# Optimization experiments

Measured on AMD Instinct MI355X. Metric: run time of the kernel, lower is better.

## Reference

```python
import jax, jax.numpy as jnp
import numpy as np

N = 50000      # nodes
E = 400000     # edges
IN = 64        # in_channels
HID = 64       # hidden_channels
H = 4          # num_heads
LAT = 32       # latent_dim
NEG_SLOPE = 0.2


def setup_inputs() -> dict:
    key = jax.random.key(0)
    ks = jax.random.split(key, 20)
    w = lambda k, shape, s=0.05: (jax.random.normal(k, shape, jnp.float32) * s)
    inp = {
        'x': jax.random.normal(ks[0], (N, IN), jnp.float32),
        'edge_index': jax.random.randint(ks[1], (2, E), 0, N, dtype=jnp.int32),
        'batch': jnp.zeros((N,), jnp.int32),
        'eps': jax.random.normal(ks[2], (N, LAT), jnp.float32),
        # conv1: in -> HID per head, 4 heads, concat
        'W1': w(ks[3], (IN, H * HID)), 'a_src1': w(ks[4], (H, HID)), 'a_dst1': w(ks[5], (H, HID)), 'b1': jnp.zeros((H * HID,), jnp.float32),
        # conv2: H*HID -> HID per head, concat
        'W2': w(ks[6], (H * HID, H * HID)), 'a_src2': w(ks[7], (H, HID)), 'a_dst2': w(ks[8], (H, HID)), 'b2': jnp.zeros((H * HID,), jnp.float32),
        # conv_mu / conv_logvar: H*HID -> LAT, 1 head, no concat
        'Wmu': w(ks[9], (H * HID, LAT)), 'a_src_mu': w(ks[10], (1, LAT)), 'a_dst_mu': w(ks[11], (1, LAT)), 'b_mu': jnp.zeros((LAT,), jnp.float32),
        'Wlv': w(ks[12], (H * HID, LAT)), 'a_src_lv': w(ks[13], (1, LAT)), 'a_dst_lv': w(ks[14], (1, LAT)), 'b_lv': jnp.zeros((LAT,), jnp.float32),
        # decoder
        'W_fc': w(ks[15], (LAT, HID)), 'b_fc': jnp.zeros((HID,), jnp.float32),
        'W_node': w(ks[16], (HID, IN)), 'b_node': jnp.zeros((IN,), jnp.float32),
        'W_edge': w(ks[17], (HID, 1)), 'b_edge': jnp.zeros((1,), jnp.float32),
    }
    return inp


def gat_layer(x, W, a_src, a_dst, b, src, dst, concat):
    """PyG-style GATConv: gather -> leaky_relu score -> per-dst softmax -> scatter-add."""
    n = x.shape[0]
    heads, c = a_src.shape
    h = (x @ W).reshape(n, heads, c)                     # [N,H,C]
    s_src = jnp.einsum('nhc,hc->nh', h, a_src)           # [N,H]
    s_dst = jnp.einsum('nhc,hc->nh', h, a_dst)
    e = jax.nn.leaky_relu(s_src[src] + s_dst[dst], NEG_SLOPE)   # [E,H]
    m = jax.ops.segment_max(e, dst, num_segments=n)      # stable softmax per destination
    e = jnp.exp(e - m[dst])
    denom = jax.ops.segment_sum(e, dst, num_segments=n)
    alpha = e / (denom[dst] + 1e-16)                     # [E,H]
    out = jax.ops.segment_sum(alpha[:, :, None] * h[src], dst, num_segments=n)  # [N,H,C]
    out = out.reshape(n, heads * c) if concat else out.mean(axis=1)
    return out + b


def reference(x, edge_index, batch, eps,
              W1, a_src1, a_dst1, b1,
              W2, a_src2, a_dst2, b2,
              Wmu, a_src_mu, a_dst_mu, b_mu,
              Wlv, a_src_lv, a_dst_lv, b_lv,
              W_fc, b_fc, W_node, b_node, W_edge, b_edge):
    n = x.shape[0]
    src0, dst0 = edge_index[0], edge_index[1]
    loops = jnp.arange(n, dtype=edge_index.dtype)        # GATConv add_self_loops=True
    src = jnp.concatenate([src0, loops])
    dst = jnp.concatenate([dst0, loops])

    # encode
    h = jax.nn.relu(gat_layer(x, W1, a_src1, a_dst1, b1, src, dst, concat=True))
    h = jax.nn.relu(gat_layer(h, W2, a_src2, a_dst2, b2, src, dst, concat=True))
    mu = gat_layer(h, Wmu, a_src_mu, a_dst_mu, b_mu, src, dst, concat=False)
    logvar = gat_layer(h, Wlv, a_src_lv, a_dst_lv, b_lv, src, dst, concat=False)

    # reparameterize (eps supplied for determinism)
    z = mu + eps * jnp.exp(0.5 * logvar)

    # decode
    zd = jax.nn.relu(z @ W_fc + b_fc)                    # [N,HID]
    node_features = zd @ W_node + b_node                 # [N,IN]
    edge_feat = zd[src0] * zd[dst0]                      # [E,HID]
    edge_scores = (edge_feat @ W_edge + b_edge).squeeze(-1)  # [E]
    return (mu, logvar, z, node_features, edge_scores)
```

## Files before the change

kernel.cpp:

```cpp
#include <hip/hip_runtime.h>
#include <math.h>

#define NEG_SLOPE 0.2f

__device__ __forceinline__ float lky(float x){ return x > 0.f ? x : NEG_SLOPE * x; }

__device__ __forceinline__ unsigned short f2bf(float f){
  unsigned int u = __float_as_uint(f);
  unsigned int r = (u + 0x7fffu + ((u >> 16) & 1u)) >> 16;
  return (unsigned short)r;
}
__device__ __forceinline__ float bf2f(unsigned short s){
  return __uint_as_float(((unsigned int)s) << 16);
}
__device__ __forceinline__ void unp8(uint4 v, float* f){
  f[0]=__uint_as_float(v.x<<16); f[1]=__uint_as_float(v.x&0xffff0000u);
  f[2]=__uint_as_float(v.y<<16); f[3]=__uint_as_float(v.y&0xffff0000u);
  f[4]=__uint_as_float(v.z<<16); f[5]=__uint_as_float(v.z&0xffff0000u);
  f[6]=__uint_as_float(v.w<<16); f[7]=__uint_as_float(v.w&0xffff0000u);
}
__device__ __forceinline__ uint4 pack8(const float* o){
  uint4 v;
  v.x = (unsigned)f2bf(o[0]) | ((unsigned)f2bf(o[1])<<16);
  v.y = (unsigned)f2bf(o[2]) | ((unsigned)f2bf(o[3])<<16);
// ... 2 lines not shown
  return v;
}

typedef __bf16 bf16x8 __attribute__((ext_vector_type(8)));
typedef float  f32x4  __attribute__((ext_vector_type(4)));
typedef float  f32x2  __attribute__((ext_vector_type(2)));

__device__ __forceinline__ uint2 pk_fp8(const float* f){
  unsigned lo = 0u, hi = 0u;
  lo = __builtin_amdgcn_cvt_pk_fp8_f32(f[0], f[1], (int)lo, false);
  lo = __builtin_amdgcn_cvt_pk_fp8_f32(f[2], f[3], (int)lo, true);
  hi = __builtin_amdgcn_cvt_pk_fp8_f32(f[4], f[5], (int)hi, false);
  hi = __builtin_amdgcn_cvt_pk_fp8_f32(f[6], f[7], (int)hi, true);
  return make_uint2(lo, hi);
}
__device__ __forceinline__ unsigned pk_fp8x4(float f0, float f1, float f2, float f3){
  unsigned u = 0u;
  u = __builtin_amdgcn_cvt_pk_fp8_f32(f0, f1, (int)u, false);
  u = __builtin_amdgcn_cvt_pk_fp8_f32(f2, f3, (int)u, true);
  return u;
}
__device__ __forceinline__ void unpk_fp8(uint2 v, float* f){
  f32x2 a0 = __builtin_amdgcn_cvt_pk_f32_fp8((int)v.x, false);
  f32x2 a1 = __builtin_amdgcn_cvt_pk_f32_fp8((int)v.x, true);
  f32x2 a2 = __builtin_amdgcn_cvt_pk_f32_fp8((int)v.y, false);
  f32x2 a3 = __builtin_amdgcn_cvt_pk_f32_fp8((int)v.y, true);
  f[0]=a0[0]; f[1]=a0[1]; f[2]=a1[0]; f[3]=a1[1];
  f[4]=a2[0]; f[5]=a2[1]; f[6]=a3[0]; f[7]=a3[1];
}

__global__ void zero_ints_kernel(int* __restrict__ p, int n){
  int i = blockIdx.x * blockDim.x + threadIdx.x;
  if (i < n) p[i] = 0;
}
__global__ void count_deg_kernel(const int* __restrict__ dst, int* __restrict__ deg, int E){
  int e = blockIdx.x * blockDim.x + threadIdx.x;
  if (e < E) atomicAdd(&deg[dst[e]], 1);
}
__global__ void scan_chunk_kernel(const int* __restrict__ deg, int* __restrict__ rowptr,
                                  int* __restrict__ bsum, int n){
  __shared__ int s[256];
  int t = threadIdx.x;
  int i = blockIdx.x * 256 + t;
  int v = (i < n) ? deg[i] : 0;
  s[t] = v; __syncthreads();
  for (int off = 1; off < 256; off <<= 1){
    int x = (t >= off) ? s[t - off] : 0;
    __syncthreads();
    s[t] += x;
    __syncthreads();
  }
  if (i < n) rowptr[i + 1] = s[t];
  if (t == 255) bsum[blockIdx.x] = s[255];
}
__global__ void scan_add_kernel(int* __restrict__ rowptr, const int* __restrict__ bsum,
                                int nb, int n){
  __shared__ int s[256];
  int t = threadIdx.x;
  int v = (t < nb) ? bsum[t] : 0;
  s[t] = v; __syncthreads();
  for (int off = 1; off < 256; off <<= 1){
    int x = (t >= off) ? s[t - off] : 0;
    __syncthreads();
    s[t] += x;
    __syncthreads();
  }
  int b = blockIdx.x;
  int excl = (b == 0) ? 0 : s[b - 1];
  int i = b * 256 + t;
  if (i < n) rowptr[i + 1] += excl;
  if (i == 0) rowptr[0] = 0;
}
__global__ void fill_csr_kernel(const int* __restrict__ src, const int* __restrict__ dst,
                                const int* __restrict__ rowptr, int* __restrict__ cursor,
                                int* __restrict__ colv, int E){
  int e = blockIdx.x * blockDim.x + threadIdx.x;
  if (e >= E) return;
  int d = dst[e];
  int pos = atomicAdd(&cursor[d], 1);
  colv[rowptr[d] + pos] = src[e];
}

__device__ __forceinline__ void pack_one(const float* Wa, const float* Wb,
                                         int K, int M, int Mhalf,
                                         unsigned short* out, int idx){
  if (idx >= K * M) return;
  int j = idx & 7;
  int l = (idx >> 3) & 63;
  int rest = idx >> 9;
  int KS = K >> 5;
  int s = rest % KS, gct = rest / KS;
  int col = gct * 16 + (l & 15);
  int k   = s * 32 + ((l >> 4) << 3) + j;
  float v;
  if (Wb == nullptr) v = Wa[(long)k * M + col];
  else v = (col < Mhalf) ? Wa[(long)k * Mhalf + col] : Wb[(long)k * Mhalf + (col - Mhalf)];
  out[idx] = f2bf(v);
}

__global__ __launch_bounds__(256) void packall_kernel(
    const float* __restrict__ W1,  unsigned short* __restrict__ W1pk,
    const float* __restrict__ W2,  unsigned short* __restrict__ W2pk,
    const float* __restrict__ Wmu, const float* __restrict__ Wlv,
    unsigned short* __restrict__ Wmvpk,
    const float* __restrict__ Wfc, unsigned short* __restrict__ Wfcpk,
    const float* __restrict__ Wnd, unsigned short* __restrict__ Wndpk,
    const float* __restrict__ as1, const float* __restrict__ ad1,
    float* __restrict__ P1)
{
  int b = blockIdx.x, t = threadIdx.x;
  if (b < 64){
    pack_one(W1, nullptr, 64, 256, 256, W1pk, b * 256 + t);
  } else if (b < 320){
    pack_one(W2, nullptr, 256, 256, 256, W2pk, (b - 64) * 256 + t);
  } else if (b < 384){
    pack_one(Wmu, Wlv, 256, 64, 32, Wmvpk, (b - 320) * 256 + t);
  } else if (b < 392){
    pack_one(Wfc, nullptr, 32, 64, 64, Wfcpk, (b - 384) * 256 + t);
  } else if (b < 408){
    pack_one(Wnd, nullptr, 64, 64, 64, Wndpk, (b - 392) * 256 + t);
  } else {
    int idx = (b - 408) * 256 + t;
    if (idx < 512){
      int sd = idx & 1, h = (idx >> 1) & 3, k = idx >> 3;
      const float* av = sd ? ad1 : as1;
      float acc = 0.f;
      for (int c = 0; c < 64; ++c) acc += W1[k * 256 + h * 64 + c] * av[h * 64 + c];
      P1[idx] = acc;
    }
  }
}

__global__ __launch_bounds__(256) void score1cvt_kernel(
    const float* __restrict__ x, const float* __restrict__ P1,
    unsigned short* __restrict__ xb,
    float* __restrict__ S1s, float* __restrict__ S1d, int n)
{
  __shared__ float P[512];
  int t = threadIdx.x;
  P[t] = P1[t]; P[t + 256] = P1[t + 256];
  __syncthreads();
  int nid = blockIdx.x * 256 + t;
  if (nid >= n) return;
  const float4* xr = (const float4*)x + (long)nid * 16;
  uint4* xw = (uint4*)xb + (long)nid * 8;
  float acc[8] = {0,0,0,0,0,0,0,0};
  for (int kc = 0; kc < 16; kc += 2){
    float4 v0 = xr[kc], v1 = xr[kc + 1];
    uint4 o;
    o.x = (unsigned)f2bf(v0.x) | ((unsigned)f2bf(v0.y) << 16);
    o.y = (unsigned)f2bf(v0.z) | ((unsigned)f2bf(v0.w) << 16);
    o.z = (unsigned)f2bf(v1.x) | ((unsigned)f2bf(v1.y) << 16);
    o.w = (unsigned)f2bf(v1.z) | ((unsigned)f2bf(v1.w) << 16);
    xw[kc >> 1] = o;
    float vf[8] = {v0.x, v0.y, v0.z, v0.w, v1.x, v1.y, v1.z, v1.w};
    #pragma unroll
    for (int j = 0; j < 8; ++j){
      int k = kc * 4 + j;
      #pragma unroll
      for (int o8 = 0; o8 < 8; ++o8) acc[o8] += vf[j] * P[k * 8 + o8];
    }
  }
  *(float4*)(S1s + nid * 4) = make_float4(acc[0], acc[2], acc[4], acc[6]);
  *(float4*)(S1d + nid * 4) = make_float4(acc[1], acc[3], acc[5], acc[7]);
}

__global__ __launch_bounds__(256) void aggx_kernel(
    const unsigned short* __restrict__ xb,
    const float* __restrict__ Ss, const float* __restrict__ Sd,
    const int* __restrict__ rowptr, const int* __restrict__ colv,
    unsigned short* __restrict__ Xagg, int n)
{
  int wv = threadIdx.x >> 6, l = threadIdx.x & 63;
  int nid = blockIdx.x * 4 + wv;
  if (nid >= n) return;
  int slot = l >> 5;
  int cl = l & 31;
  float4 sdv = *(const float4*)(Sd + (long)nid * 4);
  float acc[4][2] = {};
  float sumw[4] = {0.f, 0.f, 0.f, 0.f};
  int beg = rowptr[nid], end = rowptr[nid + 1];
  for (int jj = beg + slot; jj < end; jj += 2){
    int s = colv[jj];
    float4 a = *(const float4*)(Ss + (long)s * 4);
    float wx = __expf(lky(a.x + sdv.x));
    float wy = __expf(lky(a.y + sdv.y));
    float wz = __expf(lky(a.z + sdv.z));
    float ww = __expf(lky(a.w + sdv.w));
    unsigned xv = *((const unsigned*)xb + (long)s * 32 + cl);
    float f0 = __uint_as_float(xv << 16);
    float f1 = __uint_as_float(xv & 0xffff0000u);
    acc[0][0] += wx * f0; acc[0][1] += wx * f1;
    acc[1][0] += wy * f0; acc[1][1] += wy * f1;
    acc[2][0] += wz * f0; acc[2][1] += wz * f1;
    acc[3][0] += ww * f0; acc[3][1] += ww * f1;
    sumw[0] += wx; sumw[1] += wy; sumw[2] += wz; sumw[3] += ww;
  }
  #pragma unroll
  for (int h = 0; h < 4; ++h){
    acc[h][0] += __shfl_xor(acc[h][0], 32);
    acc[h][1] += __shfl_xor(acc[h][1], 32);
    sumw[h]   += __shfl_xor(sumw[h], 32);
  }
  float4 ssv = *(const float4*)(Ss + (long)nid * 4);
  unsigned xv = *((const unsigned*)xb + (long)nid * 32 + cl);
  float f0 = __uint_as_float(xv << 16);
  float f1 = __uint_as_float(xv & 0xffff0000u);
  float wsh[4] = { __expf(lky(ssv.x + sdv.x)), __expf(lky(ssv.y + sdv.y)),
                   __expf(lky(ssv.z + sdv.z)), __expf(lky(ssv.w + sdv.w)) };
  if (l < 32){
    #pragma unroll
    for (int h = 0; h < 4; ++h){
      float inv = 1.f / (sumw[h] + wsh[h] + 1e-16f);
      float o0 = (acc[h][0] + wsh[h] * f0) * inv;
      float o1 = (acc[h][1] + wsh[h] * f1) * inv;
      unsigned ov = (unsigned)f2bf(o0) | ((unsigned)f2bf(o1) << 16);
      *((unsigned*)Xagg + (long)nid * 128 + h * 32 + cl) = ov;
    }
  }
}

template<int K, int KB, int CW, bool BD, bool SCORES, bool RELU, bool OUT8>
__global__ __launch_bounds__(256) void gemm_mfma_kernel(
    const unsigned short* __restrict__ Xb, const unsigned short* __restrict__ Wpk,
    const float* __restrict__ a_s, const float* __restrict__ a_d,
    const float* __restrict__ a_s2, const float* __restrict__ a_d2,
    const float* __restrict__ bias,
    void* __restrict__ Hout,
    float* __restrict__ Ss, float* __restrict__ Sd,
    float* __restrict__ Ss2, float* __restrict__ Sd2, int n)
{
  constexpr int BR  = (CW == 4) ? 32 : 128;
  constexpr int M   = 64 * CW;
  constexpr int KSB = KB / 32;
  constexpr int LDA = K + 8;
  constexpr int SH  = (BR * LDA > BR * M) ? BR * LDA : BR * M;
  __shared__ unsigned short As[SH];

  const int t = threadIdx.x;
  const int w = t >> 6, l = t & 63;
  const int quad = l >> 4, l15 = l & 15;
  const long base = (long)blockIdx.x * BR;
  const int roww = (CW == 4) ? 0 : w;
  const int colw = (CW == 4) ? w : 0;
  const int abase = BD ? w * KB : 0;

  {
    const uint4* Xg = (const uint4*)Xb;
    long g0 = base * (K / 8);
    long lim = (long)n * (K / 8);
    for (int c = t; c < BR * K / 8; c += 256){
      int row = c / (K / 8), kc = c % (K / 8);
      uint4 v = make_uint4(0u, 0u, 0u, 0u);
      if (g0 + c < lim) v = Xg[g0 + c];
      *(uint4*)(As + row * LDA + kc * 8) = v;
    }
  }
  __syncthreads();

  f32x4 acc[2][4] = {};
  for (int s = 0; s < KSB; ++s){
    bf16x8 af0 = *(const bf16x8*)(As + (roww * 32 + 0  + l15) * LDA + abase + s * 32 + quad * 8);
    bf16x8 af1 = *(const bf16x8*)(As + (roww * 32 + 16 + l15) * LDA + abase + s * 32 + quad * 8);
    #pragma unroll
    for (int ct = 0; ct < 4; ++ct){
      int gct = colw * 4 + ct;
      bf16x8 bf = *(const bf16x8*)(Wpk + (((long)gct * KSB + s) * 64 + l) * 8);
      acc[0][ct] = __builtin_amdgcn_mfma_f32_16x16x32_bf16(af0, bf, acc[0][ct], 0, 0, 0);
      acc[1][ct] = __builtin_amdgcn_mfma_f32_16x16x32_bf16(af1, bf, acc[1][ct], 0, 0, 0);
    }
  }

  if constexpr (SCORES){
    if (CW == 4){
      const int head = w;
      float asv[4], adv[4];
      #pragma unroll
      for (int ct = 0; ct < 4; ++ct){
        int col = head * 64 + ct * 16 + l15;
        asv[ct] = a_s[col]; adv[ct] = a_d[col];
      }
      #pragma unroll
      for (int rt = 0; rt < 2; ++rt){
        #pragma unroll
        for (int r = 0; r < 4; ++r){
          float ps = 0.f, pd = 0.f;
          #pragma unroll
          for (int ct = 0; ct < 4; ++ct){
            float v = acc[rt][ct][r];
            ps += v * asv[ct]; pd += v * adv[ct];
          }
          ps += __shfl_xor(ps, 8); pd += __shfl_xor(pd, 8);
          ps += __shfl_xor(ps, 4); pd += __shfl_xor(pd, 4);
          ps += __shfl_xor(ps, 2); pd += __shfl_xor(pd, 2);
          ps += __shfl_xor(ps, 1); pd += __shfl_xor(pd, 1);
          long node = base + rt * 16 + quad * 4 + r;
          if (l15 == 0 && node < n){ Ss[node * 4 + head] = ps; Sd[node * 4 + head] = pd; }
        }
      }
    } else {
      float asm_[2], adm_[2], asl_[2], adl_[2];
      #pragma unroll
      for (int ct = 0; ct < 2; ++ct){
        int col = ct * 16 + l15;
        asm_[ct] = a_s[col];  adm_[ct] = a_d[col];
        asl_[ct] = a_s2[col]; adl_[ct] = a_d2[col];
      }
      #pragma unroll
      for (int rt = 0; rt < 2; ++rt){
        #pragma unroll
        for (int r = 0; r < 4; ++r){
          float psm = 0.f, pdm = 0.f, psl = 0.f, pdl = 0.f;
          #pragma unroll
          for (int ct = 0; ct < 2; ++ct){
            float vm = acc[rt][ct][r];
            float vl = acc[rt][ct + 2][r];
            psm += vm * asm_[ct]; pdm += vm * adm_[ct];
            psl += vl * asl_[ct]; pdl += vl * adl_[ct];
          }
          #pragma unroll
          for (int d = 8; d >= 1; d >>= 1){
            psm += __shfl_xor(psm, d); pdm += __shfl_xor(pdm, d);
            psl += __shfl_xor(psl, d); pdl += __shfl_xor(pdl, d);
          }
          long node = base + w * 32 + rt * 16 + quad * 4 + r;
          if (l15 == 0 && node < n){
            Ss[node]  = psm; Sd[node]  = pdm;
            Ss2[node] = psl; Sd2[node] = pdl;
          }
        }
      }
    }
  }

  __syncthreads();
  float bct[4] = {0.f, 0.f, 0.f, 0.f};
  if constexpr (RELU){
    #pragma unroll
    for (int ct = 0; ct < 4; ++ct) bct[ct] = bias[colw * 64 + ct * 16 + l15];
  }
  #pragma unroll
  for (int rt = 0; rt < 2; ++rt){
    #pragma unroll
    for (int ct = 0; ct < 4; ++ct){
      #pragma unroll
      for (int r = 0; r < 4; ++r){
        int row = roww * 32 + rt * 16 + quad * 4 + r;
        int col = colw * 64 + ct * 16 + l15;
        float o = acc[rt][ct][r];
        if constexpr (RELU) o = fmaxf(o + bct[ct], 0.f);
        int pos = col;
        if constexpr (CW == 1){ pos = (col < 32) ? (col * 2) : ((col - 32) * 2 + 1); }
        As[row * M + pos] = f2bf(o);
      }
    }
  }
  __syncthreads();
  if constexpr (OUT8){
    uint2* Hg = (uint2*)Hout;
    for (int c = t; c < BR * M / 8; c += 256){
      int row = c / (M / 8);
      uint4 v = *(const uint4*)(As + c * 8);
      float f[8]; unp8(v, f);
      if (base + row < n) Hg[base * (M / 8) + c] = pk_fp8(f);
    }
  } else {
    uint4* Hg = (uint4*)Hout;
    for (int c = t; c < BR * M / 8; c += 256){
      int row = c / (M / 8);
      if (base + row < n) Hg[base * (M / 8) + c] = *(const uint4*)(As + c * 8);
    }
  }
}

__global__ __launch_bounds__(256) void agg256_kernel(
    const unsigned char* __restrict__ H8,
    const float* __restrict__ Ss, const float* __restrict__ Sd,
    const int* __restrict__ rowptr, const int* __restrict__ colv,
    const float* __restrict__ bias, unsigned short* __restrict__ Out, int n)
{
  int wv = threadIdx.x >> 6, l = threadIdx.x & 63;
  int nid = blockIdx.x * 4 + wv;
  if (nid >= n) return;
  int slot = l >> 5;
  int cl = l & 31;
  int head = cl >> 3;
  float sdv = Sd[(long)nid * 4 + head];
  const uint2* H8v = (const uint2*)H8;
  float acc[8] = {0,0,0,0,0,0,0,0};
  float sumw = 0.f;
  int beg = rowptr[nid], end = rowptr[nid + 1];
  for (int jj = beg + slot; jj < end; jj += 2){
    int s = colv[jj];
    float wt = __expf(lky(Ss[(long)s * 4 + head] + sdv));
    uint2 hv = H8v[(long)s * 32 + cl];
    float xf[8]; unpk_fp8(hv, xf);
    #pragma unroll
    for (int j = 0; j < 8; ++j) acc[j] += wt * xf[j];
    sumw += wt;
  }
  #pragma unroll
  for (int j = 0; j < 8; ++j) acc[j] += __shfl_xor(acc[j], 32);
  sumw += __shfl_xor(sumw, 32);
  float wself = __expf(lky(Ss[(long)nid * 4 + head] + sdv));
  uint2 hv = H8v[(long)nid * 32 + cl];
  float xf[8]; unpk_fp8(hv, xf);
  if (l < 32){
    float inv = 1.f / (sumw + wself + 1e-16f);
    float4 bv0 = *(const float4*)(bias + cl * 8);
    float4 bv1 = *(const float4*)(bias + cl * 8 + 4);
    float o[8];
    o[0] = fmaxf((acc[0] + wself * xf[0]) * inv + bv0.x, 0.f);
    o[1] = fmaxf((acc[1] + wself * xf[1]) * inv + bv0.y, 0.f);
    o[2] = fmaxf((acc[2] + wself * xf[2]) * inv + bv0.z, 0.f);
    o[3] = fmaxf((acc[3] + wself * xf[3]) * inv + bv0.w, 0.f);
    o[4] = fmaxf((acc[4] + wself * xf[4]) * inv + bv1.x, 0.f);
    o[5] = fmaxf((acc[5] + wself * xf[5]) * inv + bv1.y, 0.f);
    o[6] = fmaxf((acc[6] + wself * xf[6]) * inv + bv1.z, 0.f);
    o[7] = fmaxf((acc[7] + wself * xf[7]) * inv + bv1.w, 0.f);
    *((uint4*)Out + (long)nid * 32 + cl) = pack8(o);
  }
}

__global__ __launch_bounds__(256) void agg_muv_kernel(
    const unsigned short* __restrict__ Hmuv,
    const float* __restrict__ Ssm, const float* __restrict__ Sdm,
    const float* __restrict__ Ssl, const float* __restrict__ Sdl,
    const int* __restrict__ rowptr, const int* __restrict__ colv,
    const float* __restrict__ bmu, const float* __restrict__ blv,
    const float* __restrict__ epsv,
    float* __restrict__ out_mu, float* __restrict__ out_lv, float* __restrict__ out_z,
    unsigned short* __restrict__ zb, int n)
{
  int wv = threadIdx.x >> 6, l = threadIdx.x & 63;
  int nid = blockIdx.x * 4 + wv;
  if (nid >= n) return;
  int slot = l >> 5;
  int cl = l & 31;
  float sdm = Sdm[nid], sdl = Sdl[nid];
  const unsigned* Hm32 = (const unsigned*)Hmuv;
  float am = 0.f, al = 0.f, summ = 0.f, suml = 0.f;
  int beg = rowptr[nid], end = rowptr[nid + 1];
  for (int jj = beg + slot; jj < end; jj += 2){
    int s = colv[jj];
    float wm = __expf(lky(Ssm[s] + sdm));
    float wl = __expf(lky(Ssl[s] + sdl));
    unsigned hv = Hm32[(long)s * 32 + cl];
    float mu = __uint_as_float(hv << 16);
    float lv = __uint_as_float(hv & 0xffff0000u);
    am += wm * mu; al += wl * lv;
    summ += wm; suml += wl;
  }
  am += __shfl_xor(am, 32); al += __shfl_xor(al, 32);
  summ += __shfl_xor(summ, 32); suml += __shfl_xor(suml, 32);
  float wms = __expf(lky(Ssm[nid] + sdm));
  float wls = __expf(lky(Ssl[nid] + sdl));
  unsigned hv = Hm32[(long)nid * 32 + cl];
  float mus = __uint_as_float(hv << 16);
  float lvs = __uint_as_float(hv & 0xffff0000u);
  if (l < 32){
    float mu = (am + wms * mus) / (summ + wms + 1e-16f) + bmu[cl];
    float lv = (al + wls * lvs) / (suml + wls + 1e-16f) + blv[cl];
    float z  = mu + epsv[(long)nid * 32 + cl] * expf(0.5f * lv);
    out_mu[(long)nid * 32 + cl] = mu;
    out_lv[(long)nid * 32 + cl] = lv;
    out_z [(long)nid * 32 + cl] = z;
    zb[(long)nid * 32 + cl] = f2bf(z);
  }
}

__global__ __launch_bounds__(256) void decoder_mfma_kernel(
    const unsigned short* __restrict__ zb,
    const unsigned short* __restrict__ Wfcpk, const float* __restrict__ bfc,
    const unsigned short* __restrict__ Wndpk, const float* __restrict__ bnode,
    unsigned char* __restrict__ ZD8, float* __restrict__ NF, int n)
{
  constexpr int LDA = 40;
  constexpr int LDZ = 72;
  __shared__ unsigned short As[128 * LDA];
  __shared__ unsigned short Zs[128 * LDZ];
  const int t = threadIdx.x;
  const int w = t >> 6, l = t & 63;
  const int quad = l >> 4, l15 = l & 15;
  const long base = (long)blockIdx.x * 128;

  {
    const uint4* Zg = (const uint4*)zb;
    long g0 = base * 4;
    long lim = (long)n * 4;
    for (int c = t; c < 512; c += 256){
      int row = c >> 2, kc = c & 3;
      uint4 v = make_uint4(0u, 0u, 0u, 0u);
      if (g0 + c < lim) v = Zg[g0 + c];
      *(uint4*)(As + row * LDA + kc * 8) = v;
    }
  }
  __syncthreads();

  f32x4 acc[2][4] = {};
  {
// ... 99 lines not shown
  const float* W2    = (const float*)d_in[8];
  const float* as2   = (const float*)d_in[9];
  const float* ad2   = (const float*)d_in[10];
  const float* b2    = (const float*)d_in[11];
  const float* Wmu   = (const float*)d_in[12];
  const float* asmu  = (const float*)d_in[13];
  const float* admu  = (const float*)d_in[14];
  const float* bmu   = (const float*)d_in[15];
  const float* Wlv   = (const float*)d_in[16];
  const float* aslv  = (const float*)d_in[17];
  const float* adlv  = (const float*)d_in[18];
  const float* blv   = (const float*)d_in[19];
  const float* Wfc   = (const float*)d_in[20];
  const float* bfc   = (const float*)d_in[21];
  const float* Wnode = (const float*)d_in[22];
  const float* bnode = (const float*)d_in[23];
  const float* Wedge = (const float*)d_in[24];
  const float* bedge = (const float*)d_in[25];

  const int N = in_sizes[0] / 64;
  const int E = in_sizes[1] / 2;
  const int* srcA = ei;
  const int* dstA = ei + E;

  char* wsb = (char*)d_ws;
  size_t off = 0;
  auto alloc = [&](size_t bytes) -> void* {
    void* p = wsb + off;
    off += (bytes + 255) & ~(size_t)255;
    return p;
  };
  unsigned short* xb    = (unsigned short*)alloc((size_t)N * 64 * 2);
  unsigned short* bufP  = (unsigned short*)alloc((size_t)N * 256 * 2);
  unsigned short* bufQ  = (unsigned short*)alloc((size_t)N * 256 * 2);
  unsigned char*  H8    = (unsigned char*) alloc((size_t)N * 256);
  unsigned short* Hmuv  = (unsigned short*)alloc((size_t)N * 64 * 2);
  unsigned char*  ZD8   = (unsigned char*) alloc((size_t)N * 64);
  unsigned short* zbb   = (unsigned short*)alloc((size_t)N * 32 * 2);
  unsigned short* W1pk  = (unsigned short*)alloc((size_t)64 * 256 * 2);
  unsigned short* W2pk  = (unsigned short*)alloc((size_t)256 * 256 * 2);
  unsigned short* Wmvpk = (unsigned short*)alloc((size_t)256 * 64 * 2);
  unsigned short* Wfcpk = (unsigned short*)alloc((size_t)32 * 64 * 2);
  unsigned short* Wndpk = (unsigned short*)alloc((size_t)64 * 64 * 2);
  float* P1    = (float*)alloc(512 * 4);
  float* S1s   = (float*)alloc((size_t)N * 4 * 4);
  float* S1d   = (float*)alloc((size_t)N * 4 * 4);
  float* S2s   = (float*)alloc((size_t)N * 4 * 4);
  float* S2d   = (float*)alloc((size_t)N * 4 * 4);
  float* Ssm   = (float*)alloc((size_t)N * 4);
  float* Sdm   = (float*)alloc((size_t)N * 4);
  float* Ssl   = (float*)alloc((size_t)N * 4);
  float* Sdl   = (float*)alloc((size_t)N * 4);
  int*   deg   = (int*)  alloc((size_t)N * 2 * 4);
  int*   cursor= deg + N;
  int*   rowptr= (int*)  alloc((size_t)(N + 1) * 4);
  int*   colv  = (int*)  alloc((size_t)E * 4);
  int*   bsum  = (int*)  alloc(1024);
  (void)ws_size; (void)n_in; (void)out_size;

  float* out_mu = (float*)d_out;
  float* out_lv = out_mu + (size_t)N * 32;
  float* out_z  = out_lv + (size_t)N * 32;
  float* out_nf = out_z  + (size_t)N * 32;
  float* out_es = out_nf + (size_t)N * 64;

  const int nb = (N + 255) / 256;

  zero_ints_kernel<<<(2 * N + 255) / 256, 256, 0, stream>>>(deg, 2 * N);
  count_deg_kernel<<<(E + 255) / 256, 256, 0, stream>>>(dstA, deg, E);
  scan_chunk_kernel<<<nb, 256, 0, stream>>>(deg, rowptr, bsum, N);
  scan_add_kernel<<<nb, 256, 0, stream>>>(rowptr, bsum, nb, N);
  fill_csr_kernel<<<(E + 255) / 256, 256, 0, stream>>>(srcA, dstA, rowptr, cursor, colv, E);

  packall_kernel<<<410, 256, 0, stream>>>(W1, W1pk, W2, W2pk, Wmu, Wlv, Wmvpk,
                                          Wfc, Wfcpk, Wnode, Wndpk, as1, ad1, P1);

  score1cvt_kernel<<<(N + 255) / 256, 256, 0, stream>>>(x, P1, xb, S1s, S1d, N);
  aggx_kernel<<<(N + 3) / 4, 256, 0, stream>>>(xb, S1s, S1d, rowptr, colv, bufP, N);
  gemm_mfma_kernel<256, 64, 4, true, false, true, false><<<(N + 31) / 32, 256, 0, stream>>>(
      bufP, W1pk, nullptr, nullptr, nullptr, nullptr, b1, bufQ,
      nullptr, nullptr, nullptr, nullptr, N);

  gemm_mfma_kernel<256, 256, 4, false, true, false, true><<<(N + 31) / 32, 256, 0, stream>>>(
      bufQ, W2pk, as2, ad2, nullptr, nullptr, nullptr, H8,
      S2s, S2d, nullptr, nullptr, N);
  agg256_kernel<<<(N + 3) / 4, 256, 0, stream>>>(H8, S2s, S2d, rowptr, colv, b2, bufP, N);

  gemm_mfma_kernel<256, 256, 1, false, true, false, false><<<(N + 127) / 128, 256, 0, stream>>>(
      bufP, Wmvpk, asmu, admu, aslv, adlv, nullptr, Hmuv,
      Ssm, Sdm, Ssl, Sdl, N);
  agg_muv_kernel<<<(N + 3) / 4, 256, 0, stream>>>(
      Hmuv, Ssm, Sdm, Ssl, Sdl, rowptr, colv, bmu, blv, epsv,
      out_mu, out_lv, out_z, zbb, N);

  decoder_mfma_kernel<<<(N + 127) / 128, 256, 0, stream>>>(
      zbb, Wfcpk, bfc, Wndpk, bnode, ZD8, out_nf, N);
  {
    long waves = ((long)E + 7) / 8;
    long blocks = (waves + 3) / 4;
    edge_score_kernel<<<(int)blocks, 256, 0, stream>>>(ZD8, srcA, dstA, Wedge, bedge, out_es, E);
  }
}
```

Measured before the change: 354.3 us.

## Fuse setup kernels, fuse layer-1/layer-2 GEMMs, widen aggregation lanes

Degree counting, weight packing, P1 projection and the x conversion/scoring are merged into one launch, and cursor zeroing moves into scan_add. The two layer GEMMs become one kernel that keeps the relu(XW1+b1) tile in LDS, so the bufQ round trip through global memory goes away. The aggregation kernels now use 4 edge slots of 16 lanes with wider loads instead of 2 slots of 32 lanes. This cuts launches and memory traffic, at the cost of recomputing P1 in every scoring block and adding extra shuffle reductions.

```diff
diff --git a/kernel.cpp b/kernel.cpp
--- a/kernel.cpp
+++ b/kernel.cpp
@@ -58,10 +58,6 @@
 __global__ void zero_ints_kernel(int* __restrict__ p, int n){
   int i = blockIdx.x * blockDim.x + threadIdx.x;
   if (i < n) p[i] = 0;
-}
-__global__ void count_deg_kernel(const int* __restrict__ dst, int* __restrict__ deg, int E){
-  int e = blockIdx.x * blockDim.x + threadIdx.x;
-  if (e < E) atomicAdd(&deg[dst[e]], 1);
 }
 __global__ void scan_chunk_kernel(const int* __restrict__ deg, int* __restrict__ rowptr,
                                   int* __restrict__ bsum, int n){
@@ -80,7 +76,7 @@
   if (t == 255) bsum[blockIdx.x] = s[255];
 }
 __global__ void scan_add_kernel(int* __restrict__ rowptr, const int* __restrict__ bsum,
-                                int nb, int n){
+                                int* __restrict__ cursor, int nb, int n){
   __shared__ int s[256];
   int t = threadIdx.x;
   int v = (t < nb) ? bsum[t] : 0;
@@ -94,7 +90,7 @@
   int b = blockIdx.x;
   int excl = (b == 0) ? 0 : s[b - 1];
   int i = b * 256 + t;
-  if (i < n) rowptr[i + 1] += excl;
+  if (i < n){ rowptr[i + 1] += excl; cursor[i] = 0; }
   if (i == 0) rowptr[0] = 0;
 }
 __global__ void fill_csr_kernel(const int* __restrict__ src, const int* __restrict__ dst,
@@ -124,7 +120,8 @@
   out[idx] = f2bf(v);
 }
 
-__global__ __launch_bounds__(256) void packall_kernel(
+__global__ __launch_bounds__(256) void mega_kernel(
+    const int* __restrict__ dstA, int* __restrict__ deg, int E, int nbE,
     const float* __restrict__ W1,  unsigned short* __restrict__ W1pk,
     const float* __restrict__ W2,  unsigned short* __restrict__ W2pk,
     const float* __restrict__ Wmu, const float* __restrict__ Wlv,
@@ -132,41 +129,37 @@
     const float* __restrict__ Wfc, unsigned short* __restrict__ Wfcpk,
     const float* __restrict__ Wnd, unsigned short* __restrict__ Wndpk,
     const float* __restrict__ as1, const float* __restrict__ ad1,
-    float* __restrict__ P1)
+    const float* __restrict__ x, unsigned short* __restrict__ xb,
+    float* __restrict__ S1s, float* __restrict__ S1d, int n)
 {
   int b = blockIdx.x, t = threadIdx.x;
-  if (b < 64){
-    pack_one(W1, nullptr, 64, 256, 256, W1pk, b * 256 + t);
-  } else if (b < 320){
-    pack_one(W2, nullptr, 256, 256, 256, W2pk, (b - 64) * 256 + t);
-  } else if (b < 384){
-    pack_one(Wmu, Wlv, 256, 64, 32, Wmvpk, (b - 320) * 256 + t);
-  } else if (b < 392){
-    pack_one(Wfc, nullptr, 32, 64, 64, Wfcpk, (b - 384) * 256 + t);
-  } else if (b < 408){
-    pack_one(Wnd, nullptr, 64, 64, 64, Wndpk, (b - 392) * 256 + t);
-  } else {
-    int idx = (b - 408) * 256 + t;
-    if (idx < 512){
-      int sd = idx & 1, h = (idx >> 1) & 3, k = idx >> 3;
-      const float* av = sd ? ad1 : as1;
-      float acc = 0.f;
-      for (int c = 0; c < 64; ++c) acc += W1[k * 256 + h * 64 + c] * av[h * 64 + c];
-      P1[idx] = acc;
-    }
-  }
-}
-
-__global__ __launch_bounds__(256) void score1cvt_kernel(
-    const float* __restrict__ x, const float* __restrict__ P1,
-    unsigned short* __restrict__ xb,
-    float* __restrict__ S1s, float* __restrict__ S1d, int n)
-{
+  if (b < nbE){
+    int e = b * 256 + t;
+    if (e < E) atomicAdd(&deg[dstA[e]], 1);
+    return;
+  }
+  b -= nbE;
+  if (b < 408){
+    if (b < 64)       pack_one(W1, nullptr, 64, 256, 256, W1pk, b * 256 + t);
+    else if (b < 320) pack_one(W2, nullptr, 256, 256, 256, W2pk, (b - 64) * 256 + t);
+    else if (b < 384) pack_one(Wmu, Wlv, 256, 64, 32, Wmvpk, (b - 320) * 256 + t);
+    else if (b < 392) pack_one(Wfc, nullptr, 32, 64, 64, Wfcpk, (b - 384) * 256 + t);
+    else              pack_one(Wnd, nullptr, 64, 64, 64, Wndpk, (b - 392) * 256 + t);
+    return;
+  }
+  b -= 408;
   __shared__ float P[512];
-  int t = threadIdx.x;
-  P[t] = P1[t]; P[t + 256] = P1[t + 256];
+  #pragma unroll
+  for (int rep = 0; rep < 2; ++rep){
+    int idx = t + rep * 256;
+    int sd = idx & 1, h = (idx >> 1) & 3, k = idx >> 3;
+    const float* av = sd ? ad1 : as1;
+    float acc = 0.f;
+    for (int c = 0; c < 64; ++c) acc += W1[k * 256 + h * 64 + c] * av[h * 64 + c];
+    P[idx] = acc;
+  }
   __syncthreads();
-  int nid = blockIdx.x * 256 + t;
+  int nid = b * 256 + t;
   if (nid >= n) return;
   const float4* xr = (const float4*)x + (long)nid * 16;
   uint4* xw = (uint4*)xb + (long)nid * 8;
@@ -200,49 +193,235 @@
   int wv = threadIdx.x >> 6, l = threadIdx.x & 63;
   int nid = blockIdx.x * 4 + wv;
   if (nid >= n) return;
-  int slot = l >> 5;
-  int cl = l & 31;
+  int slot = l >> 4;
+  int cl = l & 15;
   float4 sdv = *(const float4*)(Sd + (long)nid * 4);
-  float acc[4][2] = {};
+  const uint2* xb2 = (const uint2*)xb;
+  float acc[4][4] = {};
   float sumw[4] = {0.f, 0.f, 0.f, 0.f};
   int beg = rowptr[nid], end = rowptr[nid + 1];
-  for (int jj = beg + slot; jj < end; jj += 2){
+  for (int jj = beg + slot; jj < end; jj += 4){
     int s = colv[jj];
     float4 a = *(const float4*)(Ss + (long)s * 4);
     float wx = __expf(lky(a.x + sdv.x));
     float wy = __expf(lky(a.y + sdv.y));
     float wz = __expf(lky(a.z + sdv.z));
     float ww = __expf(lky(a.w + sdv.w));
-    unsigned xv = *((const unsigned*)xb + (long)s * 32 + cl);
-    float f0 = __uint_as_float(xv << 16);
-    float f1 = __uint_as_float(xv & 0xffff0000u);
-    acc[0][0] += wx * f0; acc[0][1] += wx * f1;
-    acc[1][0] += wy * f0; acc[1][1] += wy * f1;
-    acc[2][0] += wz * f0; acc[2][1] += wz * f1;
-    acc[3][0] += ww * f0; acc[3][1] += ww * f1;
+    uint2 xv = xb2[(long)s * 16 + cl];
+    float f0 = __uint_as_float(xv.x << 16);
+    float f1 = __uint_as_float(xv.x & 0xffff0000u);
+    float f2 = __uint_as_float(xv.y << 16);
+    float f3 = __uint_as_float(xv.y & 0xffff0000u);
+    acc[0][0] += wx*f0; acc[0][1] += wx*f1; acc[0][2] += wx*f2; acc[0][3] += wx*f3;
+    acc[1][0] += wy*f0; acc[1][1] += wy*f1; acc[1][2] += wy*f2; acc[1][3] += wy*f3;
+    acc[2][0] += wz*f0; acc[2][1] += wz*f1; acc[2][2] += wz*f2; acc[2][3] += wz*f3;
+    acc[3][0] += ww*f0; acc[3][1] += ww*f1; acc[3][2] += ww*f2; acc[3][3] += ww*f3;
     sumw[0] += wx; sumw[1] += wy; sumw[2] += wz; sumw[3] += ww;
   }
   #pragma unroll
-  for (int h = 0; h < 4; ++h){
-    acc[h][0] += __shfl_xor(acc[h][0], 32);
-    acc[h][1] += __shfl_xor(acc[h][1], 32);
-    sumw[h]   += __shfl_xor(sumw[h], 32);
+  for (int d = 16; d <= 32; d <<= 1){
+    #pragma unroll
+    for (int h = 0; h < 4; ++h){
+      #pragma unroll
+      for (int j = 0; j < 4; ++j) acc[h][j] += __shfl_xor(acc[h][j], d);
+      sumw[h] += __shfl_xor(sumw[h], d);
+    }
   }
   float4 ssv = *(const float4*)(Ss + (long)nid * 4);
-  unsigned xv = *((const unsigned*)xb + (long)nid * 32 + cl);
-  float f0 = __uint_as_float(xv << 16);
-  float f1 = __uint_as_float(xv & 0xffff0000u);
+  uint2 xv = xb2[(long)nid * 16 + cl];
+  float f0 = __uint_as_float(xv.x << 16);
+  float f1 = __uint_as_float(xv.x & 0xffff0000u);
+  float f2 = __uint_as_float(xv.y << 16);
+  float f3 = __uint_as_float(xv.y & 0xffff0000u);
   float wsh[4] = { __expf(lky(ssv.x + sdv.x)), __expf(lky(ssv.y + sdv.y)),
                    __expf(lky(ssv.z + sdv.z)), __expf(lky(ssv.w + sdv.w)) };
-  if (l < 32){
+  if (l < 16){
+    uint2* Xo = (uint2*)Xagg;
     #pragma unroll
     for (int h = 0; h < 4; ++h){
       float inv = 1.f / (sumw[h] + wsh[h] + 1e-16f);
       float o0 = (acc[h][0] + wsh[h] * f0) * inv;
       float o1 = (acc[h][1] + wsh[h] * f1) * inv;
-      unsigned ov = (unsigned)f2bf(o0) | ((unsigned)f2bf(o1) << 16);
-      *((unsigned*)Xagg + (long)nid * 128 + h * 32 + cl) = ov;
-    }
+      float o2 = (acc[h][2] + wsh[h] * f2) * inv;
+      float o3 = (acc[h][3] + wsh[h] * f3) * inv;
+      uint2 ov;
+      ov.x = (unsigned)f2bf(o0) | ((unsigned)f2bf(o1) << 16);
+      ov.y = (unsigned)f2bf(o2) | ((unsigned)f2bf(o3) << 16);
+      Xo[(long)nid * 64 + h * 16 + cl] = ov;
+    }
+  }
+}
+
+__global__ __launch_bounds__(256) void gemm12_kernel(
+    const unsigned short* __restrict__ Xagg,
+    const unsigned short* __restrict__ W1pk, const unsigned short* __restrict__ W2pk,
+    const float* __restrict__ b1,
+    const float* __restrict__ a_s, const float* __restrict__ a_d,
+    unsigned char* __restrict__ H8,
+    float* __restrict__ Ss, float* __restrict__ Sd, int n)
+{
+  constexpr int LDA = 264;
+  __shared__ unsigned short As[32 * LDA];
+  __shared__ unsigned short Bs[32 * LDA];
+  const int t = threadIdx.x;
+  const int w = t >> 6, l = t & 63;
+  const int quad = l >> 4, l15 = l & 15;
+  const long base = (long)blockIdx.x * 32;
+
+  {
+    const uint4* Xg = (const uint4*)Xagg;
+    long g0 = base * 32;
+    long lim = (long)n * 32;
+    for (int c = t; c < 1024; c += 256){
+      int row = c >> 5, kc = c & 31;
+      uint4 v = make_uint4(0u, 0u, 0u, 0u);
+      if (g0 + c < lim) v = Xg[g0 + c];
+      *(uint4*)(As + row * LDA + kc * 8) = v;
+    }
+  }
+  __syncthreads();
+
+  f32x4 acc1[2][4] = {};
+  const int abase = w * 64;
+  #pragma unroll
+  for (int s = 0; s < 2; ++s){
+    bf16x8 af0 = *(const bf16x8*)(As + (0  + l15) * LDA + abase + s * 32 + quad * 8);
+    bf16x8 af1 = *(const bf16x8*)(As + (16 + l15) * LDA + abase + s * 32 + quad * 8);
+    #pragma unroll
+    for (int ct = 0; ct < 4; ++ct){
+      int gct = w * 4 + ct;
+      bf16x8 bf = *(const bf16x8*)(W1pk + (((long)gct * 2 + s) * 64 + l) * 8);
+      acc1[0][ct] = __builtin_amdgcn_mfma_f32_16x16x32_bf16(af0, bf, acc1[0][ct], 0, 0, 0);
+      acc1[1][ct] = __builtin_amdgcn_mfma_f32_16x16x32_bf16(af1, bf, acc1[1][ct], 0, 0, 0);
+    }
+  }
+  #pragma unroll
+  for (int rt = 0; rt < 2; ++rt){
+    #pragma unroll
+    for (int ct = 0; ct < 4; ++ct){
+      float b = b1[w * 64 + ct * 16 + l15];
+      #pragma unroll
+      for (int r = 0; r < 4; ++r){
+        int row = rt * 16 + quad * 4 + r;
+        Bs[row * LDA + w * 64 + ct * 16 + l15] = f2bf(fmaxf(acc1[rt][ct][r] + b, 0.f));
+      }
+    }
+  }
+  __syncthreads();
+
+  f32x4 acc[2][4] = {};
+  for (int s = 0; s < 8; ++s){
+    bf16x8 af0 = *(const bf16x8*)(Bs + (0  + l15) * LDA + s * 32 + quad * 8);
+    bf16x8 af1 = *(const bf16x8*)(Bs + (16 + l15) * LDA + s * 32 + quad * 8);
+    #pragma unroll
+    for (int ct = 0; ct < 4; ++ct){
+      int gct = w * 4 + ct;
+      bf16x8 bf = *(const bf16x8*)(W2pk + (((long)gct * 8 + s) * 64 + l) * 8);
+      acc[0][ct] = __builtin_amdgcn_mfma_f32_16x16x32_bf16(af0, bf, acc[0][ct], 0, 0, 0);
+      acc[1][ct] = __builtin_amdgcn_mfma_f32_16x16x32_bf16(af1, bf, acc[1][ct], 0, 0, 0);
+    }
+  }
+
+  {
+    float asv[4], adv[4];
+    #pragma unroll
+    for (int ct = 0; ct < 4; ++ct){
+      int col = w * 64 + ct * 16 + l15;
+      asv[ct] = a_s[col]; adv[ct] = a_d[col];
+    }
+    #pragma unroll
+    for (int rt = 0; rt < 2; ++rt){
+      #pragma unroll
+      for (int r = 0; r < 4; ++r){
+        float ps = 0.f, pd = 0.f;
+        #pragma unroll
+        for (int ct = 0; ct < 4; ++ct){
+          float v = acc[rt][ct][r];
+          ps += v * asv[ct]; pd += v * adv[ct];
+        }
+        ps += __shfl_xor(ps, 8); pd += __shfl_xor(pd, 8);
+        ps += __shfl_xor(ps, 4); pd += __shfl_xor(pd, 4);
+        ps += __shfl_xor(ps, 2); pd += __shfl_xor(pd, 2);
+        ps += __shfl_xor(ps, 1); pd += __shfl_xor(pd, 1);
+        long node = base + rt * 16 + quad * 4 + r;
+        if (l15 == 0 && node < n){ Ss[node * 4 + w] = ps; Sd[node * 4 + w] = pd; }
+      }
+    }
+  }
+
+  #pragma unroll
+  for (int rt = 0; rt < 2; ++rt){
+    #pragma unroll
+    for (int ct = 0; ct < 4; ++ct){
+      #pragma unroll
+      for (int r = 0; r < 4; ++r){
+        int row = rt * 16 + quad * 4 + r;
+        As[row * 256 + w * 64 + ct * 16 + l15] = f2bf(acc[rt][ct][r]);
+      }
+    }
+  }
+  __syncthreads();
+  {
+    uint2* Hg = (uint2*)H8;
+    for (int c = t; c < 1024; c += 256){
+      int row = c >> 5;
+      uint4 v = *(const uint4*)(As + c * 8);
+      float f[8]; unp8(v, f);
+      if (base + row < n) Hg[base * 32 + c] = pk_fp8(f);
+    }
+  }
+}
+
+__global__ __launch_bounds__(256) void agg256_kernel(
+    const unsigned char* __restrict__ H8,
+    const float* __restrict__ Ss, const float* __restrict__ Sd,
+    const int* __restrict__ rowptr, const int* __restrict__ colv,
+    const float* __restrict__ bias, unsigned short* __restrict__ Out, int n)
+{
+  int wv = threadIdx.x >> 6, l = threadIdx.x & 63;
+  int nid = blockIdx.x * 4 + wv;
+  if (nid >= n) return;
+  int slot = l >> 4;
+  int cl = l & 15;
+  int head = cl >> 2;
+  float sdv = Sd[(long)nid * 4 + head];
+  const uint4* H8v = (const uint4*)H8;
+  float acc[16] = {0,0,0,0,0,0,0,0,0,0,0,0,0,0,0,0};
+  float sumw = 0.f;
+  int beg = rowptr[nid], end = rowptr[nid + 1];
+  for (int jj = beg + slot; jj < end; jj += 4){
+    int s = colv[jj];
+    float wt = __expf(lky(Ss[(long)s * 4 + head] + sdv));
+    uint4 hv = H8v[(long)s * 16 + cl];
+    float xf[16];
+    unpk_fp8(make_uint2(hv.x, hv.y), xf);
+    unpk_fp8(make_uint2(hv.z, hv.w), xf + 8);
+    #pragma unroll
+    for (int j = 0; j < 16; ++j) acc[j] += wt * xf[j];
+    sumw += wt;
+  }
+  #pragma unroll
+  for (int d = 16; d <= 32; d <<= 1){
+    #pragma unroll
+    for (int j = 0; j < 16; ++j) acc[j] += __shfl_xor(acc[j], d);
+    sumw += __shfl_xor(sumw, d);
+  }
+  float wself = __expf(lky(Ss[(long)nid * 4 + head] + sdv));
+  uint4 hv = H8v[(long)nid * 16 + cl];
+  float xf[16];
+  unpk_fp8(make_uint2(hv.x, hv.y), xf);
+  unpk_fp8(make_uint2(hv.z, hv.w), xf + 8);
+  if (l < 16){
+    float inv = 1.f / (sumw + wself + 1e-16f);
+    float o[16];
+    #pragma unroll
+    for (int j = 0; j < 16; ++j){
+      float b = bias[cl * 16 + j];
+      o[j] = fmaxf((acc[j] + wself * xf[j]) * inv + b, 0.f);
+    }
+    uint4* Og = (uint4*)Out;
+    Og[(long)nid * 32 + cl * 2]     = pack8(o);
+    Og[(long)nid * 32 + cl * 2 + 1] = pack8(o + 8);
   }
 }
 
@@ -298,73 +477,40 @@
   }
 
   if constexpr (SCORES){
-    if (CW == 4){
-      const int head = w;
-      float asv[4], adv[4];
+    float asm_[2], adm_[2], asl_[2], adl_[2];
+    #pragma unroll
+    for (int ct = 0; ct < 2; ++ct){
+      int col = ct * 16 + l15;
+      asm_[ct] = a_s[col];  adm_[ct] = a_d[col];
+      asl_[ct] = a_s2[col]; adl_[ct] = a_d2[col];
+    }
+    #pragma unroll
+    for (int rt = 0; rt < 2; ++rt){
       #pragma unroll
-      for (int ct = 0; ct < 4; ++ct){
-        int col = head * 64 + ct * 16 + l15;
-        asv[ct] = a_s[col]; adv[ct] = a_d[col];
-      }
-      #pragma unroll
-      for (int rt = 0; rt < 2; ++rt){
+      for (int r = 0; r < 4; ++r){
+        float psm = 0.f, pdm = 0.f, psl = 0.f, pdl = 0.f;
         #pragma unroll
-        for (int r = 0; r < 4; ++r){
-          float ps = 0.f, pd = 0.f;
-          #pragma unroll
-          for (int ct = 0; ct < 4; ++ct){
-            float v = acc[rt][ct][r];
-            ps += v * asv[ct]; pd += v * adv[ct];
-          }
-          ps += __shfl_xor(ps, 8); pd += __shfl_xor(pd, 8);
-          ps += __shfl_xor(ps, 4); pd += __shfl_xor(pd, 4);
-          ps += __shfl_xor(ps, 2); pd += __shfl_xor(pd, 2);
-          ps += __shfl_xor(ps, 1); pd += __shfl_xor(pd, 1);
-          long node = base + rt * 16 + quad * 4 + r;
-          if (l15 == 0 && node < n){ Ss[node * 4 + head] = ps; Sd[node * 4 + head] = pd; }
+        for (int ct = 0; ct < 2; ++ct){
+          float vm = acc[rt][ct][r];
+          float vl = acc[rt][ct + 2][r];
+          psm += vm * asm_[ct]; pdm += vm * adm_[ct];
+          psl += vl * asl_[ct]; pdl += vl * adl_[ct];
+        }
+        #pragma unroll
+        for (int d = 8; d >= 1; d >>= 1){
+          psm += __shfl_xor(psm, d); pdm += __shfl_xor(pdm, d);
+          psl += __shfl_xor(psl, d); pdl += __shfl_xor(pdl, d);
+        }
+        long node = base + w * 32 + rt * 16 + quad * 4 + r;
+        if (l15 == 0 && node < n){
+          Ss[node]  = psm; Sd[node]  = pdm;
+          Ss2[node] = psl; Sd2[node] = pdl;
         }
       }
-    } else {
-      float asm_[2], adm_[2], asl_[2], adl_[2];
-      #pragma unroll
-      for (int ct = 0; ct < 2; ++ct){
-        int col = ct * 16 + l15;
-        asm_[ct] = a_s[col];  adm_[ct] = a_d[col];
-        asl_[ct] = a_s2[col]; adl_[ct] = a_d2[col];
-      }
-      #pragma unroll
-      for (int rt = 0; rt < 2; ++rt){
-        #pragma unroll
-        for (int r = 0; r < 4; ++r){
-          float psm = 0.f, pdm = 0.f, psl = 0.f, pdl = 0.f;
-          #pragma unroll
-          for (int ct = 0; ct < 2; ++ct){
-            float vm = acc[rt][ct][r];
-            float vl = acc[rt][ct + 2][r];
-            psm += vm * asm_[ct]; pdm += vm * adm_[ct];
-            psl += vl * asl_[ct]; pdl += vl * adl_[ct];
-          }
-          #pragma unroll
-          for (int d = 8; d >= 1; d >>= 1){
-            psm += __shfl_xor(psm, d); pdm += __shfl_xor(pdm, d);
-            psl += __shfl_xor(psl, d); pdl += __shfl_xor(pdl, d);
-          }
-          long node = base + w * 32 + rt * 16 + quad * 4 + r;
-          if (l15 == 0 && node < n){
-            Ss[node]  = psm; Sd[node]  = pdm;
-            Ss2[node] = psl; Sd2[node] = pdl;
-          }
-        }
-      }
     }
   }
 
   __syncthreads();
-  float bct[4] = {0.f, 0.f, 0.f, 0.f};
-  if constexpr (RELU){
-    #pragma unroll
-    for (int ct = 0; ct < 4; ++ct) bct[ct] = bias[colw * 64 + ct * 16 + l15];
-  }
   #pragma unroll
   for (int rt = 0; rt < 2; ++rt){
     #pragma unroll
@@ -374,7 +520,6 @@
         int row = roww * 32 + rt * 16 + quad * 4 + r;
         int col = colw * 64 + ct * 16 + l15;
         float o = acc[rt][ct][r];
-        if constexpr (RELU) o = fmaxf(o + bct[ct], 0.f);
         int pos = col;
         if constexpr (CW == 1){ pos = (col < 32) ? (col * 2) : ((col - 32) * 2 + 1); }
         As[row * M + pos] = f2bf(o);
@@ -382,69 +527,12 @@
     }
   }
   __syncthreads();
-  if constexpr (OUT8){
-    uint2* Hg = (uint2*)Hout;
-    for (int c = t; c < BR * M / 8; c += 256){
-      int row = c / (M / 8);
-      uint4 v = *(const uint4*)(As + c * 8);
-      float f[8]; unp8(v, f);
-      if (base + row < n) Hg[base * (M / 8) + c] = pk_fp8(f);
-    }
-  } else {
+  {
     uint4* Hg = (uint4*)Hout;
     for (int c = t; c < BR * M / 8; c += 256){
       int row = c / (M / 8);
       if (base + row < n) Hg[base * (M / 8) + c] = *(const uint4*)(As + c * 8);
     }
-  }
-}
-
-__global__ __launch_bounds__(256) void agg256_kernel(
-    const unsigned char* __restrict__ H8,
-    const float* __restrict__ Ss, const float* __restrict__ Sd,
-    const int* __restrict__ rowptr, const int* __restrict__ colv,
-    const float* __restrict__ bias, unsigned short* __restrict__ Out, int n)
-{
-  int wv = threadIdx.x >> 6, l = threadIdx.x & 63;
-  int nid = blockIdx.x * 4 + wv;
-  if (nid >= n) return;
-  int slot = l >> 5;
-  int cl = l & 31;
-  int head = cl >> 3;
-  float sdv = Sd[(long)nid * 4 + head];
-  const uint2* H8v = (const uint2*)H8;
-  float acc[8] = {0,0,0,0,0,0,0,0};
-  float sumw = 0.f;
-  int beg = rowptr[nid], end = rowptr[nid + 1];
-  for (int jj = beg + slot; jj < end; jj += 2){
-    int s = colv[jj];
-    float wt = __expf(lky(Ss[(long)s * 4 + head] + sdv));
-    uint2 hv = H8v[(long)s * 32 + cl];
-    float xf[8]; unpk_fp8(hv, xf);
-    #pragma unroll
-    for (int j = 0; j < 8; ++j) acc[j] += wt * xf[j];
-    sumw += wt;
-  }
-  #pragma unroll
-  for (int j = 0; j < 8; ++j) acc[j] += __shfl_xor(acc[j], 32);
-  sumw += __shfl_xor(sumw, 32);
-  float wself = __expf(lky(Ss[(long)nid * 4 + head] + sdv));
-  uint2 hv = H8v[(long)nid * 32 + cl];
-  float xf[8]; unpk_fp8(hv, xf);
-  if (l < 32){
-    float inv = 1.f / (sumw + wself + 1e-16f);
-    float4 bv0 = *(const float4*)(bias + cl * 8);
-    float4 bv1 = *(const float4*)(bias + cl * 8 + 4);
-    float o[8];
-    o[0] = fmaxf((acc[0] + wself * xf[0]) * inv + bv0.x, 0.f);
-    o[1] = fmaxf((acc[1] + wself * xf[1]) * inv + bv0.y, 0.f);
-    o[2] = fmaxf((acc[2] + wself * xf[2]) * inv + bv0.z, 0.f);
-    o[3] = fmaxf((acc[3] + wself * xf[3]) * inv + bv0.w, 0.f);
-    o[4] = fmaxf((acc[4] + wself * xf[4]) * inv + bv1.x, 0.f);
-    o[5] = fmaxf((acc[5] + wself * xf[5]) * inv + bv1.y, 0.f);
-    o[6] = fmaxf((acc[6] + wself * xf[6]) * inv + bv1.z, 0.f);
-    o[7] = fmaxf((acc[7] + wself * xf[7]) * inv + bv1.w, 0.f);
-    *((uint4*)Out + (long)nid * 32 + cl) = pack8(o);
   }
 }
 
@@ -461,37 +549,51 @@
   int wv = threadIdx.x >> 6, l = threadIdx.x & 63;
   int nid = blockIdx.x * 4 + wv;
   if (nid >= n) return;
-  int slot = l >> 5;
-  int cl = l & 31;
+  int slot = l >> 4;
+  int cl = l & 15;
   float sdm = Sdm[nid], sdl = Sdl[nid];
-  const unsigned* Hm32 = (const unsigned*)Hmuv;
-  float am = 0.f, al = 0.f, summ = 0.f, suml = 0.f;
+  const uint2* Hm2 = (const uint2*)Hmuv;
+  float am0 = 0.f, al0 = 0.f, am1 = 0.f, al1 = 0.f, summ = 0.f, suml = 0.f;
   int beg = rowptr[nid], end = rowptr[nid + 1];
-  for (int jj = beg + slot; jj < end; jj += 2){
+  for (int jj = beg + slot; jj < end; jj += 4){
     int s = colv[jj];
     float wm = __expf(lky(Ssm[s] + sdm));
     float wl = __expf(lky(Ssl[s] + sdl));
-    unsigned hv = Hm32[(long)s * 32 + cl];
-    float mu = __uint_as_float(hv << 16);
-    float lv = __uint_as_float(hv & 0xffff0000u);
-    am += wm * mu; al += wl * lv;
+    uint2 hv = Hm2[(long)s * 16 + cl];
+    am0 += wm * __uint_as_float(hv.x << 16);
+    al0 += wl * __uint_as_float(hv.x & 0xffff0000u);
+    am1 += wm * __uint_as_float(hv.y << 16);
+    al1 += wl * __uint_as_float(hv.y & 0xffff0000u);
     summ += wm; suml += wl;
   }
-  am += __shfl_xor(am, 32); al += __shfl_xor(al, 32);
-  summ += __shfl_xor(summ, 32); suml += __shfl_xor(suml, 32);
+  #pragma unroll
+  for (int d = 16; d <= 32; d <<= 1){
+    am0 += __shfl_xor(am0, d); al0 += __shfl_xor(al0, d);
+    am1 += __shfl_xor(am1, d); al1 += __shfl_xor(al1, d);
+    summ += __shfl_xor(summ, d); suml += __shfl_xor(suml, d);
+  }
   float wms = __expf(lky(Ssm[nid] + sdm));
   float wls = __expf(lky(Ssl[nid] + sdl));
-  unsigned hv = Hm32[(long)nid * 32 + cl];
-  float mus = __uint_as_float(hv << 16);
-  float lvs = __uint_as_float(hv & 0xffff0000u);
-  if (l < 32){
-    float mu = (am + wms * mus) / (summ + wms + 1e-16f) + bmu[cl];
-    float lv = (al + wls * lvs) / (suml + wls + 1e-16f) + blv[cl];
-    float z  = mu + epsv[(long)nid * 32 + cl] * expf(0.5f * lv);
-    out_mu[(long)nid * 32 + cl] = mu;
-    out_lv[(long)nid * 32 + cl] = lv;
-    out_z [(long)nid * 32 + cl] = z;
-    zb[(long)nid * 32 + cl] = f2bf(z);
+  uint2 hv = Hm2[(long)nid * 16 + cl];
+  float mus0 = __uint_as_float(hv.x << 16);
+  float lvs0 = __uint_as_float(hv.x & 0xffff0000u);
+  float mus1 = __uint_as_float(hv.y << 16);
+  float lvs1 = __uint_as_float(hv.y & 0xffff0000u);
+  if (l < 16){
+    int c0 = cl * 2;
+    float invm = 1.f / (summ + wms + 1e-16f);
+    float invl = 1.f / (suml + wls + 1e-16f);
+    float mu0 = (am0 + wms * mus0) * invm + bmu[c0];
+    float lv0 = (al0 + wls * lvs0) * invl + blv[c0];
+    float mu1 = (am1 + wms * mus1) * invm + bmu[c0 + 1];
+    float lv1 = (al1 + wls * lvs1) * invl + blv[c0 + 1];
+    float2 ev = *(const float2*)(epsv + (long)nid * 32 + c0);
+    float z0 = mu0 + ev.x * expf(0.5f * lv0);
+    float z1 = mu1 + ev.y * expf(0.5f * lv1);
+    *(float2*)(out_mu + (long)nid * 32 + c0) = make_float2(mu0, mu1);
+    *(float2*)(out_lv + (long)nid * 32 + c0) = make_float2(lv0, lv1);
+    *(float2*)(out_z  + (long)nid * 32 + c0) = make_float2(z0, z1);
+    *((unsigned*)zb + (long)nid * 16 + cl) = (unsigned)f2bf(z0) | ((unsigned)f2bf(z1) << 16);
   }
 }
 
@@ -657,7 +759,6 @@
   };
   unsigned short* xb    = (unsigned short*)alloc((size_t)N * 64 * 2);
   unsigned short* bufP  = (unsigned short*)alloc((size_t)N * 256 * 2);
-  unsigned short* bufQ  = (unsigned short*)alloc((size_t)N * 256 * 2);
   unsigned char*  H8    = (unsigned char*) alloc((size_t)N * 256);
   unsigned short* Hmuv  = (unsigned short*)alloc((size_t)N * 64 * 2);
   unsigned char*  ZD8   = (unsigned char*) alloc((size_t)N * 64);
@@ -667,7 +768,6 @@
   unsigned short* Wmvpk = (unsigned short*)alloc((size_t)256 * 64 * 2);
   unsigned short* Wfcpk = (unsigned short*)alloc((size_t)32 * 64 * 2);
   unsigned short* Wndpk = (unsigned short*)alloc((size_t)64 * 64 * 2);
-  float* P1    = (float*)alloc(512 * 4);
   float* S1s   = (float*)alloc((size_t)N * 4 * 4);
   float* S1d   = (float*)alloc((size_t)N * 4 * 4);
   float* S2s   = (float*)alloc((size_t)N * 4 * 4);
@@ -676,8 +776,8 @@
   float* Sdm   = (float*)alloc((size_t)N * 4);
   float* Ssl   = (float*)alloc((size_t)N * 4);
   float* Sdl   = (float*)alloc((size_t)N * 4);
-  int*   deg   = (int*)  alloc((size_t)N * 2 * 4);
-  int*   cursor= deg + N;
+  int*   deg   = (int*)  alloc((size_t)N * 4);
+  int*   cursor= (int*)  alloc((size_t)N * 4);
   int*   rowptr= (int*)  alloc((size_t)(N + 1) * 4);
   int*   colv  = (int*)  alloc((size_t)E * 4);
   int*   bsum  = (int*)  alloc(1024);
@@ -689,26 +789,21 @@
   float* out_nf = out_z  + (size_t)N * 32;
   float* out_es = out_nf + (size_t)N * 64;
 
-  const int nb = (N + 255) / 256;
-
-  zero_ints_kernel<<<(2 * N + 255) / 256, 256, 0, stream>>>(deg, 2 * N);
-  count_deg_kernel<<<(E + 255) / 256, 256, 0, stream>>>(dstA, deg, E);
+  const int nb  = (N + 255) / 256;
+  const int nbE = (E + 255) / 256;
+
+  zero_ints_kernel<<<nb, 256, 0, stream>>>(deg, N);
+  mega_kernel<<<nbE + 408 + nb, 256, 0, stream>>>(
+      dstA, deg, E, nbE,
+      W1, W1pk, W2, W2pk, Wmu, Wlv, Wmvpk, Wfc, Wfcpk, Wnode, Wndpk,
+      as1, ad1, x, xb, S1s, S1d, N);
   scan_chunk_kernel<<<nb, 256, 0, stream>>>(deg, rowptr, bsum, N);
-  scan_add_kernel<<<nb, 256, 0, stream>>>(rowptr, bsum, nb, N);
-  fill_csr_kernel<<<(E + 255) / 256, 256, 0, stream>>>(srcA, dstA, rowptr, cursor, colv, E);
-
-  packall_kernel<<<410, 256, 0, stream>>>(W1, W1pk, W2, W2pk, Wmu, Wlv, Wmvpk,
-                                          Wfc, Wfcpk, Wnode, Wndpk, as1, ad1, P1);
-
-  score1cvt_kernel<<<(N + 255) / 256, 256, 0, stream>>>(x, P1, xb, S1s, S1d, N);
+  scan_add_kernel<<<nb, 256, 0, stream>>>(rowptr, bsum, cursor, nb, N);
+  fill_csr_kernel<<<nbE, 256, 0, stream>>>(srcA, dstA, rowptr, cursor, colv, E);
+
   aggx_kernel<<<(N + 3) / 4, 256, 0, stream>>>(xb, S1s, S1d, rowptr, colv, bufP, N);
-  gemm_mfma_kernel<256, 64, 4, true, false, true, false><<<(N + 31) / 32, 256, 0, stream>>>(
-      bufP, W1pk, nullptr, nullptr, nullptr, nullptr, b1, bufQ,
-      nullptr, nullptr, nullptr, nullptr, N);
-
-  gemm_mfma_kernel<256, 256, 4, false, true, false, true><<<(N + 31) / 32, 256, 0, stream>>>(
-      bufQ, W2pk, as2, ad2, nullptr, nullptr, nullptr, H8,
-      S2s, S2d, nullptr, nullptr, N);
+  gemm12_kernel<<<(N + 31) / 32, 256, 0, stream>>>(
+      bufP, W1pk, W2pk, b1, as2, ad2, H8, S2s, S2d, N);
   agg256_kernel<<<(N + 3) / 4, 256, 0, stream>>>(H8, S2s, S2d, rowptr, colv, b2, bufP, N);
 
   gemm_mfma_kernel<256, 256, 1, false, true, false, false><<<(N + 127) / 128, 256, 0, stream>>>(
```

Measured after the change: 337.1 us. 1.05x faster.
